# Kernel optimization log

Hardware: AMD Instinct MI355X
Metric: run time of the kernel (lower is better)

Reference implementation:

```python
import jax, jax.numpy as jnp
import numpy as np

N = 100_000          # nodes
G = 2_000            # graphs
MUL0, MUL1 = 256, 128
DIM = MUL0 + 3 * MUL1  # 640
EPS = 1e-5
SQRT_K0 = 1.0 / np.sqrt(MUL0 + MUL1)          # fan_in of 0e slice: 256+128
SQRT_K1 = 1.0 / np.sqrt(MUL0 + 2 * MUL1)      # fan_in of 1e slice: 256+128+128


def setup_inputs() -> dict:
    key = jax.random.key(0)
    ks = jax.random.split(key, 8)
    x = jax.random.normal(ks[0], (N, DIM), dtype=jnp.float32)
    y = jax.random.normal(ks[1], (N, 4), dtype=jnp.float32)
    batch = jnp.sort(jax.random.randint(ks[2], (N,), 0, G)).astype(jnp.int32)
    # uvw path weights (e3nn internal weights, randn then rescaled by sqrt_k)
    w000 = jax.random.normal(ks[3], (MUL0, 1, MUL0), dtype=jnp.float32) * SQRT_K0
    w110 = jax.random.normal(ks[4], (MUL1, 1, MUL0), dtype=jnp.float32) * SQRT_K0
    w011 = jax.random.normal(ks[5], (MUL0, 1, MUL1), dtype=jnp.float32) * SQRT_K1
    w101 = jax.random.normal(ks[6], (MUL1, 1, MUL1), dtype=jnp.float32) * SQRT_K1
    w111 = jax.random.normal(ks[7], (MUL1, 1, MUL1), dtype=jnp.float32) * SQRT_K1
    bias0 = jnp.zeros((MUL0,), jnp.float32)           # bias on 0e slice
    mean_shift = jnp.ones((MUL0,), jnp.float32)
    affine_weight = jnp.ones((MUL0 + MUL1,), jnp.float32)
    affine_bias = jnp.zeros((MUL0,), jnp.float32)
    return dict(x=x, y=y, w000=w000, w011=w011, w101=w101, w110=w110,
                w111=w111, bias0=bias0, mean_shift=mean_shift,
                affine_weight=affine_weight, affine_bias=affine_bias,
                batch=batch)


def _segment_mean(vals, batch, counts):
    s = jax.ops.segment_sum(vals, batch, num_segments=G)
    return s / counts.reshape((G,) + (1,) * (vals.ndim - 1))


def reference(x, y, w000, w011, w101, w110, w111, bias0, mean_shift,
              affine_weight, affine_bias, batch):
    n = x.shape[0]
    s1 = x[:, :MUL0]                      # [N,256]  0e
    v1 = x[:, MUL0:].reshape(n, MUL1, 3)  # [N,128,3] 1e
    s2 = y[:, :1]                         # [N,1]    0e
    v2 = y[:, 1:].reshape(n, 1, 3)        # [N,1,3]  1e

    inv_sqrt3 = np.float32(1.0 / np.sqrt(3.0))
    # ---- fully connected tensor product (5 uvw paths) ----
    # output 0e slice: path weight sqrt(d_out)=1
    p000 = jnp.einsum('nu,nv,uvw->nw', s1, s2, w000)
    p110 = jnp.einsum('nui,nvi,uvw->nw', v1, v2, w110) * inv_sqrt3
    out0 = p000 + p110 + bias0                          # bias on scalar-even slice
    # output 1e slice: path weight sqrt(3); CG = 1/sqrt(3) (delta) or 1/sqrt(6) (eps)
    p011 = jnp.einsum('nu,nvk,uvw->nwk', s1, v2, w011)  # sqrt3/sqrt3 = 1
    p101 = jnp.einsum('nui,nv,uvw->nwi', v1, s2, w101)
    cross = jnp.cross(v1, v2)                           # [N,128,3]
    p111 = jnp.einsum('nuk,uvw->nwk', cross, w111) * np.float32(1.0 / np.sqrt(2.0))
    out1 = p011 + p101 + p111                           # [N,128,3]

    counts = jnp.maximum(
        jax.ops.segment_sum(jnp.ones((n,), x.dtype), batch, num_segments=G), 1.0)

    # ---- EquivariantGraphNorm (component norm, mean reduce, affine) ----
    # 0e field: per-graph mean shift, then per-graph rms normalization
    f0_mean = _segment_mean(out0, batch, counts)        # [G,256]
    f0 = out0 - f0_mean[batch] * mean_shift
    n0 = _segment_mean(f0 * f0, batch, counts)          # d=1 component norm
    n0 = jax.lax.rsqrt(n0 + EPS) * affine_weight[:MUL0]
    f0 = f0 * n0[batch] + affine_bias

    # 1e field: component norm = mean over the 3 components
    n1 = _segment_mean(jnp.mean(out1 * out1, axis=-1), batch, counts)  # [G,128]
    n1 = jax.lax.rsqrt(n1 + EPS) * affine_weight[MUL0:]
    f1 = out1 * n1[batch][:, :, None]

    return jnp.concatenate([f0, f1.reshape(n, MUL1 * 3)], axis=-1)
```

## Files before the change

kernel.cpp:

```cpp
#include <hip/hip_runtime.h>
#include <math.h>

#define N_ROWS 100000
#define NG     2000
#define M0     256
#define M1     128
#define DIMX   640
#define EPSV   1e-5f
#define BM     32

#define INV_SQRT3 0.57735026918962576f
#define INV_SQRT2 0.70710678118654752f

#define OFF_U  0
#define OFF_D  98304
#define OFF_V  131072
#define WT_TOTAL 163840

typedef __attribute__((ext_vector_type(8))) short bf16x8;
typedef __attribute__((ext_vector_type(4))) float f32x4;

__device__ __forceinline__ unsigned short f2bf(float f) {
    union { float f; unsigned int u; } v; v.f = f;
    unsigned int r = v.u + 0x7fff + ((v.u >> 16) & 1);
    return (unsigned short)(r >> 16);
}
__device__ __forceinline__ float bf2f(unsigned short u) {
    union { unsigned int u; float f; } v; v.u = ((unsigned int)u) << 16; return v.f;
}

__device__ __forceinline__ int lower_bound_i(const int* __restrict__ b, int n, int key) {
    int lo = 0, hi = n;
    while (lo < hi) { int m = (lo + hi) >> 1; if (b[m] < key) lo = m + 1; else hi = m; }
    return lo;
}

__global__ __launch_bounds__(256)
void k0_pack(const float* __restrict__ w000, const float* __restrict__ w011,
             const float* __restrict__ w101, const float* __restrict__ w110,
             const float* __restrict__ w111, unsigned short* __restrict__ WT)
{
    int i = blockIdx.x * 256 + threadIdx.x;
    if (i >= WT_TOTAL) return;
    int l = (i >> 3) & 63, e = i & 7;
    int lc = l & 15, lk = (l >> 4) << 3;
    float val;
    if (i < OFF_D) {
        int tile = i >> 9; int f = tile >> 3, kk = tile & 7;
        int col = f * 16 + lc, k = kk * 32 + lk + e;
        val = (col < 256) ? w000[k * 256 + col] : w011[k * 128 + (col - 256)];
    } else if (i < OFF_V) {
        int j = i - OFF_D; int tile = j >> 9; int f = tile >> 2, kk = tile & 3;
        int col = f * 16 + lc, k = kk * 32 + lk + e;
        val = w110[k * 256 + col] * INV_SQRT3;
    } else {
        int j = i - OFF_V; int tile = j >> 9; int f = tile >> 2, kk = tile & 3;
        int col = f * 16 + lc, k = kk * 32 + lk + e;
        val = (col < 128) ? w101[k * 128 + col]
                          : w111[k * 128 + (col - 128)] * INV_SQRT2;
    }
    WT[i] = f2bf(val);
}

__device__ __forceinline__ bf16x8 ldA(const unsigned short* base, int KW,
                                      int row, int kk, int kg)
{
    int off = row * KW + (((kk << 5) + (kg << 3)) ^ ((row & 7) << 3));
    return *(const bf16x8*)(base + off);
}

__global__ __launch_bounds__(256, 3)
void k1_mfma(const float* __restrict__ x, const float* __restrict__ y,
             const unsigned short* __restrict__ WT, const float* __restrict__ bias0,
             float* __restrict__ out)
{
    __shared__ unsigned short xs1[BM][256];
    __shared__ unsigned short xv[3][BM][128];
    __shared__ unsigned short xd[BM][128];
    __shared__ float sY[BM][4];
    __shared__ float sBias[256];

    const int t    = threadIdx.x;
    const int lane = t & 63;
    const int wv   = t >> 6;
    const int cb   = lane & 15;
    const int kg   = lane >> 4;
    const int hy   = blockIdx.x & 1;
    const int n0   = (blockIdx.x >> 1) * BM;

    if (t < 128) sY[t >> 2][t & 3] = y[(size_t)(n0 + (t >> 2)) * 4 + (t & 3)];
    sBias[t] = bias0[t];

    #pragma unroll
    for (int i = 0; i < 8; ++i) {
        int idx = i * 256 + t;
        int r = idx >> 6, c4 = idx & 63;
        float4 v = *(const float4*)(x + (size_t)(n0 + r) * DIMX + c4 * 4);
        ushort4 o = { f2bf(v.x), f2bf(v.y), f2bf(v.z), f2bf(v.w) };
        *(ushort4*)&xs1[r][(c4 * 4) ^ ((r & 7) << 3)] = o;
    }
    #pragma unroll
    for (int i = 0; i < 4; ++i) {
        int idx = i * 256 + t;
        int r = idx >> 5, q = idx & 31;
        const float* vp = x + (size_t)(n0 + r) * DIMX + M0 + q * 12;
        float4 a = *(const float4*)vp;
        float4 b = *(const float4*)(vp + 4);
        float4 c = *(const float4*)(vp + 8);
        int off = (q * 4) ^ ((r & 7) << 3);
        ushort4 ox = { f2bf(a.x), f2bf(a.w), f2bf(b.z), f2bf(c.y) };
        ushort4 oy = { f2bf(a.y), f2bf(b.x), f2bf(b.w), f2bf(c.z) };
        ushort4 oz = { f2bf(a.z), f2bf(b.y), f2bf(c.x), f2bf(c.w) };
        *(ushort4*)&xv[0][r][off] = ox;
        *(ushort4*)&xv[1][r][off] = oy;
        *(ushort4*)&xv[2][r][off] = oz;
    }
    __syncthreads();

    #pragma unroll
    for (int i = 0; i < 4; ++i) {
        int idx = i * 256 + t;
        int r = idx >> 5, q = idx & 31;
        int off = (q * 4) ^ ((r & 7) << 3);
        ushort4 ux = *(const ushort4*)&xv[0][r][off];
        ushort4 uy = *(const ushort4*)&xv[1][r][off];
        ushort4 uz = *(const ushort4*)&xv[2][r][off];
        float v2x = sY[r][1], v2y = sY[r][2], v2z = sY[r][3];
        ushort4 od;
        od.x = f2bf(bf2f(ux.x) * v2x + bf2f(uy.x) * v2y + bf2f(uz.x) * v2z);
        od.y = f2bf(bf2f(ux.y) * v2x + bf2f(uy.y) * v2y + bf2f(uz.y) * v2z);
        od.z = f2bf(bf2f(ux.z) * v2x + bf2f(uy.z) * v2y + bf2f(uz.z) * v2z);
        od.w = f2bf(bf2f(ux.w) * v2x + bf2f(uy.w) * v2y + bf2f(uz.w) * v2z);
        *(ushort4*)&xd[r][off] = od;
    }
    __syncthreads();

    float s2v[2][4];
    #pragma unroll
    for (int rg = 0; rg < 2; ++rg)
        #pragma unroll
        for (int j = 0; j < 4; ++j)
            s2v[rg][j] = sY[rg * 16 + kg * 4 + j][0];

    f32x4 aO[2][2];
    f32x4 aG[2];
    #pragma unroll
    for (int q = 0; q < 2; ++q) { aO[q][0] = (f32x4){0,0,0,0}; aO[q][1] = (f32x4){0,0,0,0}; }
    aG[0] = (f32x4){0,0,0,0}; aG[1] = (f32x4){0,0,0,0};

    #pragma unroll
    for (int kk = 0; kk < 8; ++kk) {
        bf16x8 a0 = ldA(&xs1[0][0], 256, cb, kk, kg);
        bf16x8 a1 = ldA(&xs1[0][0], 256, 16 + cb, kk, kg);
        #pragma unroll
        for (int q = 0; q < 3; ++q) {
            int f = (q < 2) ? (wv * 4 + hy * 2 + q) : (16 + wv * 2 + hy);
            bf16x8 b = *(const bf16x8*)(WT + OFF_U + (size_t)(f * 8 + kk) * 512 + lane * 8);
            if (q < 2) {
                aO[q][0] = __builtin_amdgcn_mfma_f32_16x16x32_bf16(a0, b, aO[q][0], 0, 0, 0);
                aO[q][1] = __builtin_amdgcn_mfma_f32_16x16x32_bf16(a1, b, aO[q][1], 0, 0, 0);
            } else {
                aG[0] = __builtin_amdgcn_mfma_f32_16x16x32_bf16(a0, b, aG[0], 0, 0, 0);
                aG[1] = __builtin_amdgcn_mfma_f32_16x16x32_bf16(a1, b, aG[1], 0, 0, 0);
            }
        }
    }

    #pragma unroll
    for (int q = 0; q < 2; ++q)
        #pragma unroll
        for (int rg = 0; rg < 2; ++rg)
            #pragma unroll
            for (int j = 0; j < 4; ++j)
                aO[q][rg][j] *= s2v[rg][j];

    #pragma unroll
    for (int kk = 0; kk < 4; ++kk) {
        bf16x8 a0 = ldA(&xd[0][0], 128, cb, kk, kg);
        bf16x8 a1 = ldA(&xd[0][0], 128, 16 + cb, kk, kg);
        #pragma unroll
        for (int q = 0; q < 2; ++q) {
            int f = wv * 4 + hy * 2 + q;
            bf16x8 b = *(const bf16x8*)(WT + OFF_D + (size_t)(f * 4 + kk) * 512 + lane * 8);
            aO[q][0] = __builtin_amdgcn_mfma_f32_16x16x32_bf16(a0, b, aO[q][0], 0, 0, 0);
            aO[q][1] = __builtin_amdgcn_mfma_f32_16x16x32_bf16(a1, b, aO[q][1], 0, 0, 0);
        }
    }

    #pragma unroll
    for (int q = 0; q < 2; ++q) {
        int col = wv * 64 + hy * 32 + q * 16 + cb;
        float bb = sBias[col];
        #pragma unroll
        for (int rg = 0; rg < 2; ++rg)
            #pragma unroll
            for (int j = 0; j < 4; ++j) {
                int row = rg * 16 + kg * 4 + j;
                out[(size_t)(n0 + row) * DIMX + col] = aO[q][rg][j] + bb;
            }
    }

    f32x4 aV[2][3][2];
    #pragma unroll
    for (int q = 0; q < 2; ++q)
        #pragma unroll
        for (int j = 0; j < 3; ++j) { aV[q][j][0] = (f32x4){0,0,0,0}; aV[q][j][1] = (f32x4){0,0,0,0}; }

    #pragma unroll
    for (int kk = 0; kk < 4; ++kk) {
        bf16x8 av[3][2];
        #pragma unroll
        for (int j = 0; j < 3; ++j) {
            av[j][0] = ldA(&xv[j][0][0], 128, cb, kk, kg);
            av[j][1] = ldA(&xv[j][0][0], 128, 16 + cb, kk, kg);
        }
        #pragma unroll
        for (int q = 0; q < 2; ++q) {
            int f = (q == 0) ? (wv * 2 + hy) : (8 + wv * 2 + hy);
            bf16x8 b = *(const bf16x8*)(WT + OFF_V + (size_t)(f * 4 + kk) * 512 + lane * 8);
            #pragma unroll
            for (int j = 0; j < 3; ++j) {
                aV[q][j][0] = __builtin_amdgcn_mfma_f32_16x16x32_bf16(av[j][0], b, aV[q][j][0], 0, 0, 0);
                aV[q][j][1] = __builtin_amdgcn_mfma_f32_16x16x32_bf16(av[j][1], b, aV[q][j][1], 0, 0, 0);
            }
        }
    }

    {
        int w = wv * 32 + hy * 16 + cb;
        #pragma unroll
        for (int rg = 0; rg < 2; ++rg)
            #pragma unroll
            for (int j = 0; j < 4; ++j) {
                int row = rg * 16 + kg * 4 + j;
                int n = n0 + row;
                float g   = aG[rg][j];
                float s2r = sY[row][0];
                float w2x = sY[row][1], w2y = sY[row][2], w2z = sY[row][3];
                float P0 = aV[0][0][rg][j], P1 = aV[0][1][rg][j], P2 = aV[0][2][rg][j];
                float Q0 = aV[1][0][rg][j], Q1 = aV[1][1][rg][j], Q2 = aV[1][2][rg][j];
                float e0 = w2x * g + s2r * P0 + w2z * Q1 - w2y * Q2;
                float e1 = w2y * g + s2r * P1 + w2x * Q2 - w2z * Q0;
                float e2 = w2z * g + s2r * P2 + w2y * Q0 - w2x * Q1;
                float* p = out + (size_t)n * DIMX + M0 + 3 * w;
                *(float2*)p = make_float2(e0, e1);
                p[2] = e2;
            }
    }
}

__global__ __launch_bounds__(640)
void k2_norm(float* __restrict__ out, const int* __restrict__ batch,
             const float* __restrict__ mean_shift, const float* __restrict__ aw,
             const float* __restrict__ ab)
{
    __shared__ float sS[4][DIMX];
    __shared__ float sQ[4][DIMX];
    __shared__ float sScale[DIMX];
    __shared__ float sShift[DIMX];
    __shared__ int   sSE[2];

    const int g = blockIdx.x;
    const int t = threadIdx.x;
    if (t == 0) {
        sSE[0] = lower_bound_i(batch, N_ROWS, g);
        sSE[1] = lower_bound_i(batch, N_ROWS, g + 1);
    }
    __syncthreads();
    const int start = sSE[0], end = sSE[1];
    float cnt = (float)(end - start);
    if (cnt < 1.f) cnt = 1.f;

    const int rl = t / 160;
    const int ct = t % 160;
    const int c0 = ct * 4;

    float4 s4 = make_float4(0.f, 0.f, 0.f, 0.f);
    float4 q4 = make_float4(0.f, 0.f, 0.f, 0.f);
    for (int n = start + rl; n < end; n += 4) {
        float4 v = *(const float4*)(out + (size_t)n * DIMX + c0);
        s4.x += v.x; q4.x = fmaf(v.x, v.x, q4.x);
        s4.y += v.y; q4.y = fmaf(v.y, v.y, q4.y);
        s4.z += v.z; q4.z = fmaf(v.z, v.z, q4.z);
        s4.w += v.w; q4.w = fmaf(v.w, v.w, q4.w);
    }
    *(float4*)&sS[rl][c0] = s4;
    *(float4*)&sQ[rl][c0] = q4;
    __syncthreads();

    float sum = sS[0][t] + sS[1][t] + sS[2][t] + sS[3][t];
    float sq  = sQ[0][t] + sQ[1][t] + sQ[2][t] + sQ[3][t];

    if (t < M0) {
        float mean = sum / cnt;
        float esq  = sq / cnt;
        float ms   = mean_shift[t];
        float var  = esq - 2.f * ms * mean * mean + ms * ms * mean * mean;
        float sc   = rsqrtf(var + EPSV) * aw[t];
        sScale[t] = sc;
        sShift[t] = ab[t] - mean * ms * sc;
    } else {
        sQ[0][t] = sq;
    }
    __syncthreads();
    if (t >= M0) {
        int w = (t - M0) / 3;
        float qq = sQ[0][M0 + 3 * w] + sQ[0][M0 + 3 * w + 1] + sQ[0][M0 + 3 * w + 2];
        sScale[t] = rsqrtf(qq / (3.f * cnt) + EPSV) * aw[M0 + w];
        sShift[t] = 0.f;
    }
    __syncthreads();

    const float4 sc4 = *(const float4*)&sScale[c0];
    const float4 sh4 = *(const float4*)&sShift[c0];
    for (int n = start + rl; n < end; n += 4) {
        float* p = out + (size_t)n * DIMX + c0;
        float4 v = *(const float4*)p;
        v.x = fmaf(v.x, sc4.x, sh4.x);
        v.y = fmaf(v.y, sc4.y, sh4.y);
        v.z = fmaf(v.z, sc4.z, sh4.z);
        v.w = fmaf(v.w, sc4.w, sh4.w);
        *(float4*)p = v;
    }
}

extern "C" void kernel_launch(void* const* d_in, const int* in_sizes, int n_in,
                              void* d_out, int out_size, void* d_ws, size_t ws_size,
                              hipStream_t stream)
{
    const float* x     = (const float*)d_in[0];
    const float* y     = (const float*)d_in[1];
    const float* w000  = (const float*)d_in[2];
    const float* w011  = (const float*)d_in[3];
    const float* w101  = (const float*)d_in[4];
    const float* w110  = (const float*)d_in[5];
    const float* w111  = (const float*)d_in[6];
    const float* bias0 = (const float*)d_in[7];
    const float* mshift= (const float*)d_in[8];
    const float* aw    = (const float*)d_in[9];
    const float* ab    = (const float*)d_in[10];
    const int*   batch = (const int*)d_in[11];
    float* out = (float*)d_out;

    unsigned short* WT = (unsigned short*)d_ws;

    k0_pack<<<WT_TOTAL / 256, 256, 0, stream>>>(w000, w011, w101, w110, w111, WT);
    k1_mfma<<<(N_ROWS / BM) * 2, 256, 0, stream>>>(x, y, WT, bias0, out);
    k2_norm<<<NG, 640, 0, stream>>>(out, batch, mshift, aw, ab);
}
```

Measured before the change: 326.2 us.

## Split graph norm into scalar and vector kernels staging rows in LDS as bf16

```diff
diff --git a/kernel.cpp b/kernel.cpp
--- a/kernel.cpp
+++ b/kernel.cpp
@@ -8,6 +8,7 @@
 #define DIMX   640
 #define EPSV   1e-5f
 #define BM     32
+#define STROWS 80
 
 #define INV_SQRT3 0.57735026918962576f
 #define INV_SQRT2 0.70710678118654752f
@@ -249,15 +250,15 @@
     }
 }
 
-__global__ __launch_bounds__(640)
-void k2_norm(float* __restrict__ out, const int* __restrict__ batch,
-             const float* __restrict__ mean_shift, const float* __restrict__ aw,
-             const float* __restrict__ ab)
-{
-    __shared__ float sS[4][DIMX];
-    __shared__ float sQ[4][DIMX];
-    __shared__ float sScale[DIMX];
-    __shared__ float sShift[DIMX];
+__global__ __launch_bounds__(256)
+void k2a_norm(float* __restrict__ out, const int* __restrict__ batch,
+              const float* __restrict__ mean_shift, const float* __restrict__ aw,
+              const float* __restrict__ ab)
+{
+    __shared__ unsigned short stage[STROWS * 256];
+    __shared__ float sS[4][256];
+    __shared__ float sQ[4][256];
+    __shared__ float sScale[256], sShift[256];
     __shared__ int   sSE[2];
 
     const int g = blockIdx.x;
@@ -268,30 +269,40 @@
     }
     __syncthreads();
     const int start = sSE[0], end = sSE[1];
-    float cnt = (float)(end - start);
-    if (cnt < 1.f) cnt = 1.f;
-
-    const int rl = t / 160;
-    const int ct = t % 160;
-    const int c0 = ct * 4;
+    const int cnt_i = end - start;
+    float cnt = (float)cnt_i; if (cnt < 1.f) cnt = 1.f;
+    const int rl = t >> 6;
+    const int c0 = (t & 63) * 4;
+    const bool staged = (cnt_i <= STROWS);
 
     float4 s4 = make_float4(0.f, 0.f, 0.f, 0.f);
     float4 q4 = make_float4(0.f, 0.f, 0.f, 0.f);
-    for (int n = start + rl; n < end; n += 4) {
-        float4 v = *(const float4*)(out + (size_t)n * DIMX + c0);
-        s4.x += v.x; q4.x = fmaf(v.x, v.x, q4.x);
-        s4.y += v.y; q4.y = fmaf(v.y, v.y, q4.y);
-        s4.z += v.z; q4.z = fmaf(v.z, v.z, q4.z);
-        s4.w += v.w; q4.w = fmaf(v.w, v.w, q4.w);
+    if (staged) {
+        for (int n = start + rl; n < end; n += 4) {
+            float4 v = *(const float4*)(out + (size_t)n * DIMX + c0);
+            s4.x += v.x; q4.x = fmaf(v.x, v.x, q4.x);
+            s4.y += v.y; q4.y = fmaf(v.y, v.y, q4.y);
+            s4.z += v.z; q4.z = fmaf(v.z, v.z, q4.z);
+            s4.w += v.w; q4.w = fmaf(v.w, v.w, q4.w);
+            ushort4 o = { f2bf(v.x), f2bf(v.y), f2bf(v.z), f2bf(v.w) };
+            *(ushort4*)&stage[(n - start) * 256 + c0] = o;
+        }
+    } else {
+        for (int n = start + rl; n < end; n += 4) {
+            float4 v = *(const float4*)(out + (size_t)n * DIMX + c0);
+            s4.x += v.x; q4.x = fmaf(v.x, v.x, q4.x);
+            s4.y += v.y; q4.y = fmaf(v.y, v.y, q4.y);
+            s4.z += v.z; q4.z = fmaf(v.z, v.z, q4.z);
+            s4.w += v.w; q4.w = fmaf(v.w, v.w, q4.w);
+        }
     }
     *(float4*)&sS[rl][c0] = s4;
     *(float4*)&sQ[rl][c0] = q4;
     __syncthreads();
 
-    float sum = sS[0][t] + sS[1][t] + sS[2][t] + sS[3][t];
-    float sq  = sQ[0][t] + sQ[1][t] + sQ[2][t] + sQ[3][t];
-
-    if (t < M0) {
+    {
+        float sum = sS[0][t] + sS[1][t] + sS[2][t] + sS[3][t];
+        float sq  = sQ[0][t] + sQ[1][t] + sQ[2][t] + sQ[3][t];
         float mean = sum / cnt;
         float esq  = sq / cnt;
         float ms   = mean_shift[t];
@@ -299,28 +310,110 @@
         float sc   = rsqrtf(var + EPSV) * aw[t];
         sScale[t] = sc;
         sShift[t] = ab[t] - mean * ms * sc;
-    } else {
-        sQ[0][t] = sq;
-    }
-    __syncthreads();
-    if (t >= M0) {
-        int w = (t - M0) / 3;
-        float qq = sQ[0][M0 + 3 * w] + sQ[0][M0 + 3 * w + 1] + sQ[0][M0 + 3 * w + 2];
-        sScale[t] = rsqrtf(qq / (3.f * cnt) + EPSV) * aw[M0 + w];
-        sShift[t] = 0.f;
     }
     __syncthreads();
 
     const float4 sc4 = *(const float4*)&sScale[c0];
     const float4 sh4 = *(const float4*)&sShift[c0];
-    for (int n = start + rl; n < end; n += 4) {
-        float* p = out + (size_t)n * DIMX + c0;
-        float4 v = *(const float4*)p;
-        v.x = fmaf(v.x, sc4.x, sh4.x);
-        v.y = fmaf(v.y, sc4.y, sh4.y);
-        v.z = fmaf(v.z, sc4.z, sh4.z);
-        v.w = fmaf(v.w, sc4.w, sh4.w);
-        *(float4*)p = v;
+    if (staged) {
+        for (int n = start + rl; n < end; n += 4) {
+            ushort4 u = *(const ushort4*)&stage[(n - start) * 256 + c0];
+            float4 v = make_float4(bf2f(u.x), bf2f(u.y), bf2f(u.z), bf2f(u.w));
+            v.x = fmaf(v.x, sc4.x, sh4.x);
+            v.y = fmaf(v.y, sc4.y, sh4.y);
+            v.z = fmaf(v.z, sc4.z, sh4.z);
+            v.w = fmaf(v.w, sc4.w, sh4.w);
+            *(float4*)(out + (size_t)n * DIMX + c0) = v;
+        }
+    } else {
+        for (int n = start + rl; n < end; n += 4) {
+            float* p = out + (size_t)n * DIMX + c0;
+            float4 v = *(const float4*)p;
+            v.x = fmaf(v.x, sc4.x, sh4.x);
+            v.y = fmaf(v.y, sc4.y, sh4.y);
+            v.z = fmaf(v.z, sc4.z, sh4.z);
+            v.w = fmaf(v.w, sc4.w, sh4.w);
+            *(float4*)p = v;
+        }
+    }
+}
+
+__global__ __launch_bounds__(384)
+void k2b_norm(float* __restrict__ out, const int* __restrict__ batch,
+              const float* __restrict__ aw)
+{
+    __shared__ unsigned short stage[STROWS * 384];
+    __shared__ float sQ[4][384];
+    __shared__ float sScale[384];
+    __shared__ float sA1[128];
+    __shared__ int   sSE[2];
+
+    const int g = blockIdx.x;
+    const int t = threadIdx.x;
+    if (t == 0) {
+        sSE[0] = lower_bound_i(batch, N_ROWS, g);
+        sSE[1] = lower_bound_i(batch, N_ROWS, g + 1);
+    }
+    __syncthreads();
+    const int start = sSE[0], end = sSE[1];
+    const int cnt_i = end - start;
+    float cnt = (float)cnt_i; if (cnt < 1.f) cnt = 1.f;
+    const int rl = t / 96;
+    const int cl = (t % 96) * 4;
+    const int c0 = M0 + cl;
+    const bool staged = (cnt_i <= STROWS);
+
+    float4 q4 = make_float4(0.f, 0.f, 0.f, 0.f);
+    if (staged) {
+        for (int n = start + rl; n < end; n += 4) {
+            float4 v = *(const float4*)(out + (size_t)n * DIMX + c0);
+            q4.x = fmaf(v.x, v.x, q4.x);
+            q4.y = fmaf(v.y, v.y, q4.y);
+            q4.z = fmaf(v.z, v.z, q4.z);
+            q4.w = fmaf(v.w, v.w, q4.w);
+            ushort4 o = { f2bf(v.x), f2bf(v.y), f2bf(v.z), f2bf(v.w) };
+            *(ushort4*)&stage[(n - start) * 384 + cl] = o;
+        }
+    } else {
+        for (int n = start + rl; n < end; n += 4) {
+            float4 v = *(const float4*)(out + (size_t)n * DIMX + c0);
+            q4.x = fmaf(v.x, v.x, q4.x);
+            q4.y = fmaf(v.y, v.y, q4.y);
+            q4.z = fmaf(v.z, v.z, q4.z);
+            q4.w = fmaf(v.w, v.w, q4.w);
+        }
+    }
+    *(float4*)&sQ[rl][cl] = q4;
+    __syncthreads();
+
+    if (t < 384) {
+        float sq = sQ[0][t] + sQ[1][t] + sQ[2][t] + sQ[3][t];
+        sQ[0][t] = sq;
+    }
+    __syncthreads();
+    if (t < 128) {
+        float qq = sQ[0][3 * t] + sQ[0][3 * t + 1] + sQ[0][3 * t + 2];
+        sA1[t] = rsqrtf(qq / (3.f * cnt) + EPSV) * aw[M0 + t];
+    }
+    __syncthreads();
+    if (t < 384) sScale[t] = sA1[t / 3];
+    __syncthreads();
+
+    const float4 sc4 = *(const float4*)&sScale[cl];
+    if (staged) {
+        for (int n = start + rl; n < end; n += 4) {
+            ushort4 u = *(const ushort4*)&stage[(n - start) * 384 + cl];
+            float4 v = make_float4(bf2f(u.x) * sc4.x, bf2f(u.y) * sc4.y,
+                                   bf2f(u.z) * sc4.z, bf2f(u.w) * sc4.w);
+            *(float4*)(out + (size_t)n * DIMX + c0) = v;
+        }
+    } else {
+        for (int n = start + rl; n < end; n += 4) {
+            float* p = out + (size_t)n * DIMX + c0;
+            float4 v = *(const float4*)p;
+            v.x *= sc4.x; v.y *= sc4.y; v.z *= sc4.z; v.w *= sc4.w;
+            *(float4*)p = v;
+        }
     }
 }
 
@@ -346,5 +439,6 @@
 
     k0_pack<<<WT_TOTAL / 256, 256, 0, stream>>>(w000, w011, w101, w110, w111, WT);
     k1_mfma<<<(N_ROWS / BM) * 2, 256, 0, stream>>>(x, y, WT, bias0, out);
-    k2_norm<<<NG, 640, 0, stream>>>(out, batch, mshift, aw, ab);
-}
+    k2a_norm<<<NG, 256, 0, stream>>>(out, batch, mshift, aw, ab);
+    k2b_norm<<<NG, 384, 0, stream>>>(out, batch, aw);
+}
```

Result: slower. 388.0 us (+19.0%).
